# Performance work log

Hardware: AMD Instinct MI355X
Metric: run time of the kernel (lower is better)

Reference implementation:

```python
import jax, jax.numpy as jnp
import numpy as np

N_HEAD = 16
DIMS = 1024

def setup_inputs() -> dict:
    key = jax.random.key(0)
    ks = jax.random.split(key, 5)
    B, T, C = 4, 2048, DIMS
    std = 1.0 / np.sqrt(C)
    x = jax.random.normal(ks[0], (B, T, C), dtype=jnp.float32)
    W_attn = jax.random.normal(ks[1], (C, 3 * C), dtype=jnp.float32) * std
    b_attn = jnp.zeros((3 * C,), dtype=jnp.float32)
    W_proj = jax.random.normal(ks[2], (C, C), dtype=jnp.float32) * std
    b_proj = jnp.zeros((C,), dtype=jnp.float32)
    return {"x": x, "W_attn": W_attn, "b_attn": b_attn, "W_proj": W_proj, "b_proj": b_proj}

def reference(x, W_attn, b_attn, W_proj, b_proj):
    B, T, C = x.shape
    H = N_HEAD
    D = C // H
    qkv = x @ W_attn + b_attn  # [B,T,3C]
    q, k, v = jnp.split(qkv, 3, axis=-1)
    # [B,T,C] -> [B,H,T,D]
    q = q.reshape(B, T, H, D).transpose(0, 2, 1, 3)
    k = k.reshape(B, T, H, D).transpose(0, 2, 1, 3)
    v = v.reshape(B, T, H, D).transpose(0, 2, 1, 3)
    att = jnp.einsum('bhqd,bhkd->bhqk', q, k) * (1.0 / np.sqrt(D))
    causal = jnp.tril(jnp.ones((T, T), dtype=bool))  # [T,T]
    att = jnp.where(causal[None, None, :, :], att, -jnp.inf)
    att = jax.nn.softmax(att, axis=-1)
    # dropout p=0.0 -> identity in eval/zero-prob mode
    y = jnp.einsum('bhqk,bhkd->bhqd', att, v)  # [B,H,T,D]
    y = y.transpose(0, 2, 1, 3).reshape(B, T, C)
    y = y @ W_proj + b_proj
    return y
```

## Files before the change

kernel.cpp:

```cpp
#include <hip/hip_runtime.h>
#include <hip/hip_bf16.h>
#include <stdint.h>

typedef unsigned short u16;
typedef unsigned int   u32;

using short8 = __attribute__((ext_vector_type(8))) short;
using f32x4  = __attribute__((ext_vector_type(4))) float;

__device__ __forceinline__ float b2f(u32 u) {
    union { u32 i; float f; } v;
    v.i = u << 16;
    return v.f;
}
__device__ __forceinline__ u16 f2b(float f) {
    union { float f; u32 i; } v; v.f = f;
    u32 x = v.i;
    x += 0x7fffu + ((x >> 16) & 1u);
    return (u16)(x >> 16);
}
__device__ __forceinline__ u32 pkbf16(float lo, float hi) {
    __hip_bfloat162 h = __float22bfloat162_rn(float2{lo, hi});
    return *reinterpret_cast<u32*>(&h);
}
__device__ __forceinline__ float fexp2(float x) {
#if __has_builtin(__builtin_amdgcn_exp2f)
    return __builtin_amdgcn_exp2f(x);
#else
    return exp2f(x);
#endif
}
__device__ __forceinline__ u32 perm_lo(u32 a, u32 b) {
#if __has_builtin(__builtin_amdgcn_perm)
    return __builtin_amdgcn_perm(b, a, 0x05040100u);
#else
    return (a & 0xffffu) | (b << 16);
#endif
}
__device__ __forceinline__ u32 perm_hi(u32 a, u32 b) {
#if __has_builtin(__builtin_amdgcn_perm)
    return __builtin_amdgcn_perm(b, a, 0x07060302u);
#else
    return (a >> 16) | (b & 0xffff0000u);
#endif
}

__device__ __forceinline__ void gll16(const u16* g, u16* l) {
    __builtin_amdgcn_global_load_lds(
        (const __attribute__((address_space(1))) void*)g,
        (__attribute__((address_space(3))) void*)l, 16, 0, 0);
}

__global__ __launch_bounds__(256)
void cast_bf16(const float* __restrict__ in, u16* __restrict__ out, int n)
{
    const int i = (blockIdx.x * 256 + threadIdx.x) * 8;
    if (i >= n) return;
    const float4 a = *reinterpret_cast<const float4*>(in + i);
    const float4 b = *reinterpret_cast<const float4*>(in + i + 4);
    *reinterpret_cast<uint4*>(out + i) = make_uint4(
        pkbf16(a.x, a.y), pkbf16(a.z, a.w), pkbf16(b.x, b.y), pkbf16(b.z, b.w));
}

__global__ __launch_bounds__(256)
void transpose_cast(const float* __restrict__ W, u16* __restrict__ Wt, int R, int Ncols)
{
    __shared__ float t[32][33];
    const int c0 = blockIdx.x * 32, r0 = blockIdx.y * 32;
    const int lx = threadIdx.x & 31, ly = threadIdx.x >> 5;
#pragma unroll
    for (int i = 0; i < 4; i++) {
        const int r = ly + i * 8;
        t[r][lx] = W[(size_t)(r0 + r) * Ncols + c0 + lx];
    }
    __syncthreads();
#pragma unroll
    for (int i = 0; i < 4; i++) {
        const int c = ly + i * 8;
        Wt[(size_t)(c0 + c) * R + r0 + lx] = f2b(t[lx][c]);
    }
}

template<typename OT>
__global__ __launch_bounds__(256)
void gemm_mfma(const u16* __restrict__ A, const u16* __restrict__ Bt,
               const float* __restrict__ bias, OT* __restrict__ C,
               int M, int N, int K)
{
    __shared__ u16 As[128 * 32];
    __shared__ u16 Bs[128 * 32];

    const int tid  = threadIdx.x;
    const int w    = tid >> 6;
    const int lane = tid & 63;
    const int quad = lane >> 4;
    const int c16  = lane & 15;
    const int wr   = w >> 1, wc = w & 1;

    const int m0 = blockIdx.y * 128;
    const int n0 = blockIdx.x * 128;

    const int srow = w * 32 + (lane >> 2);
    const int skc  = (lane & 3) * 8;
    const u16* gA = A  + (size_t)(m0 + srow) * K + skc;
    const u16* gB = Bt + (size_t)(n0 + srow) * K + skc;
    u16* lA = As + w * 32 * 32 + lane * 8;
    u16* lB = Bs + w * 32 * 32 + lane * 8;

    f32x4 acc[4][4];
#pragma unroll
    for (int i = 0; i < 4; i++)
#pragma unroll
        for (int j = 0; j < 4; j++) acc[i][j] = (f32x4){0.f, 0.f, 0.f, 0.f};

    for (int k0 = 0; k0 < K; k0 += 32) {
        __syncthreads();
        gll16(gA + k0,                  lA);
        gll16(gA + k0 + 16 * (size_t)K, lA + 16 * 32);
        gll16(gB + k0,                  lB);
        gll16(gB + k0 + 16 * (size_t)K, lB + 16 * 32);
        __syncthreads();

        short8 af[4], bf[4];
#pragma unroll
        for (int i = 0; i < 4; i++)
            af[i] = *reinterpret_cast<const short8*>(&As[(wr * 64 + i * 16 + c16) * 32 + quad * 8]);
#pragma unroll
        for (int j = 0; j < 4; j++)
            bf[j] = *reinterpret_cast<const short8*>(&Bs[(wc * 64 + j * 16 + c16) * 32 + quad * 8]);
#pragma unroll
        for (int i = 0; i < 4; i++)
#pragma unroll
            for (int j = 0; j < 4; j++)
                acc[i][j] = __builtin_amdgcn_mfma_f32_16x16x32_bf16(af[i], bf[j], acc[i][j], 0, 0, 0);
    }

#pragma unroll
    for (int i = 0; i < 4; i++)
#pragma unroll
        for (int j = 0; j < 4; j++) {
            const int colg = n0 + wc * 64 + j * 16 + c16;
            const float bv = bias[colg];
#pragma unroll
            for (int r = 0; r < 4; r++) {
                const int rowg = m0 + wr * 64 + i * 16 + quad * 4 + r;
                const float v = acc[i][j][r] + bv;
                if constexpr (sizeof(OT) == 2)
                    ((u16*)C)[(size_t)rowg * N + colg] = f2b(v);
                else
                    ((float*)C)[(size_t)rowg * N + colg] = v;
            }
        }
}

__global__ __launch_bounds__(512, 2)
void gemm_mfma_256(const u16* __restrict__ A, const u16* __restrict__ Bt,
                   const float* __restrict__ bias, u16* __restrict__ C,
                   int M, int N, int K)
{
    __shared__ u16 ring[4 * 16384];

    const int tid  = threadIdx.x;
    const int w    = tid >> 6;
    const int lane = tid & 63;
    const int quad = lane >> 4;
    const int c16  = lane & 15;
    const int wr   = w >> 2;
    const int wc   = w & 3;

    const int nwg  = gridDim.x * gridDim.y;
    const int orig = blockIdx.y * gridDim.x + blockIdx.x;
    const int swz  = (orig & 7) * (nwg >> 3) + (orig >> 3);
    const int bx   = swz % gridDim.x;
    const int by   = swz / gridDim.x;
    const int m0   = by * 256, n0 = bx * 256;

    const int r0s = w * 16 + (lane >> 2);
    const int qs  = (lane & 3) ^ ((r0s >> 1) & 3);
    const u16* gA = A  + (size_t)(m0 + r0s) * K + qs * 8;
    const u16* gB = Bt + (size_t)(n0 + r0s) * K + qs * 8;
    const size_t hstep = (size_t)128 * K;
    u16* dstB = ring + w * 512 + lane * 8;

    const int slot = quad ^ ((c16 >> 1) & 3);
    const int aoff = (wr * 128 + c16) * 32 + slot * 8;
    const int boff = 8192 + (wc * 64 + c16) * 32 + slot * 8;

    f32x4 acc[8][4];
#pragma unroll
    for (int i = 0; i < 8; i++)
#pragma unroll
        for (int j = 0; j < 4; j++) acc[i][j] = (f32x4){0.f, 0.f, 0.f, 0.f};

    const int nt = K >> 5;

#pragma unroll
    for (int t = 0; t < 3; t++) {
        u16* db = dstB + t * 16384;
        const size_t ko = (size_t)t * 32;
        gll16(gA + ko,         db);
        gll16(gA + ko + hstep, db + 4096);
        gll16(gB + ko,         db + 8192);
        gll16(gB + ko + hstep, db + 12288);
    }

#pragma unroll 1
    for (int t = 0; t < nt; t++) {
        const int remain = nt - 1 - t;
        if (remain >= 2)      asm volatile("s_waitcnt vmcnt(8)" ::: "memory");
        else if (remain == 1) asm volatile("s_waitcnt vmcnt(4)" ::: "memory");
        else                  asm volatile("s_waitcnt vmcnt(0)" ::: "memory");
        asm volatile("s_barrier" ::: "memory");

        const u16* buf = ring + (t & 3) * 16384;
        const bool pf  = (t + 3) < nt;
        u16* db = dstB + ((t + 3) & 3) * 16384;
        const size_t ko = (size_t)(t + 3) * 32;

        short8 bfr[4], afr[4];

#pragma unroll
        for (int j = 0; j < 4; j++)
            bfr[j] = *reinterpret_cast<const short8*>(buf + boff + j * 512);
#pragma unroll
        for (int i = 0; i < 4; i++)
            afr[i] = *reinterpret_cast<const short8*>(buf + aoff + i * 512);
        if (pf) { gll16(gA + ko, db); gll16(gA + ko + hstep, db + 4096); }
        asm volatile("s_waitcnt lgkmcnt(0)" ::: "memory");
        __builtin_amdgcn_sched_barrier(0);
        __builtin_amdgcn_s_setprio(1);
#pragma unroll
        for (int i = 0; i < 4; i++)
#pragma unroll
            for (int j = 0; j < 4; j++)
                acc[i][j] = __builtin_amdgcn_mfma_f32_16x16x32_bf16(afr[i], bfr[j], acc[i][j], 0, 0, 0);
        __builtin_amdgcn_s_setprio(0);
        asm volatile("s_barrier" ::: "memory");

#pragma unroll
        for (int i = 0; i < 4; i++)
            afr[i] = *reinterpret_cast<const short8*>(buf + aoff + (i + 4) * 512);
        if (pf) { gll16(gB + ko, db + 8192); gll16(gB + ko + hstep, db + 12288); }
        asm volatile("s_waitcnt lgkmcnt(0)" ::: "memory");
        __builtin_amdgcn_sched_barrier(0);
        __builtin_amdgcn_s_setprio(1);
#pragma unroll
        for (int i = 0; i < 4; i++)
#pragma unroll
            for (int j = 0; j < 4; j++)
                acc[i + 4][j] = __builtin_amdgcn_mfma_f32_16x16x32_bf16(afr[i], bfr[j], acc[i + 4][j], 0, 0, 0);
        __builtin_amdgcn_s_setprio(0);
        asm volatile("s_barrier" ::: "memory");
    }

#pragma unroll
    for (int i = 0; i < 8; i++)
#pragma unroll
        for (int j = 0; j < 4; j++) {
            const int colg = n0 + wc * 64 + j * 16 + c16;
            const float bv = bias[colg];
#pragma unroll
            for (int r = 0; r < 4; r++) {
                const int rowg = m0 + wr * 128 + i * 16 + quad * 4 + r;
                C[(size_t)rowg * N + colg] = f2b(acc[i][j][r] + bv);
            }
        }
}

constexpr int ALDP = 72;

struct TileState {
    f32x4 O[4];
    float m, l;
    short8 qf[2];
    int qglob;
};

__device__ __forceinline__ void tile_pass(
    const u16 (*__restrict__ Ks)[ALDP], const u16 (*__restrict__ Vt)[ALDP],
    u16* __restrict__ plrow,
    TileState& ts, int kt0, bool diag, int quad, int c16)
{
    f32x4 s[4];
#pragma unroll
    for (int sub = 0; sub < 4; sub++) {
        short8 kf0 = *reinterpret_cast<const short8*>(&Ks[sub * 16 + c16][0 * 32 + quad * 8]);
        short8 kf1 = *reinterpret_cast<const short8*>(&Ks[sub * 16 + c16][1 * 32 + quad * 8]);
        f32x4 acc = (f32x4){0.f, 0.f, 0.f, 0.f};
        acc = __builtin_amdgcn_mfma_f32_16x16x32_bf16(kf0, ts.qf[0], acc, 0, 0, 0);
        acc = __builtin_amdgcn_mfma_f32_16x16x32_bf16(kf1, ts.qf[1], acc, 0, 0, 0);
        s[sub] = acc;
    }

    if (diag) {
#pragma unroll
        for (int sub = 0; sub < 4; sub++)
#pragma unroll
            for (int r = 0; r < 4; r++)
                if (kt0 + sub * 16 + quad * 4 + r > ts.qglob) s[sub][r] = -INFINITY;
    }

    float mloc = -INFINITY;
#pragma unroll
    for (int sub = 0; sub < 4; sub++)
#pragma unroll
        for (int r = 0; r < 4; r++) mloc = fmaxf(mloc, s[sub][r]);
    mloc = fmaxf(mloc, __shfl_xor(mloc, 16));
    mloc = fmaxf(mloc, __shfl_xor(mloc, 32));
    const float mnew = fmaxf(ts.m, mloc);
    const float al   = fexp2(ts.m - mnew);
    ts.m = mnew;

    float ls = 0.f;
#pragma unroll
    for (int sub = 0; sub < 4; sub++) {
#pragma unroll
        for (int r = 0; r < 4; r++) {
            s[sub][r] = fexp2(s[sub][r] - mnew);
            ls += s[sub][r];
        }
        *reinterpret_cast<uint2*>(plrow + c16 * ALDP + sub * 16 + quad * 4) =
            make_uint2(pkbf16(s[sub][0], s[sub][1]), pkbf16(s[sub][2], s[sub][3]));
    }
    ls += __shfl_xor(ls, 16);
    ls += __shfl_xor(ls, 32);
    ts.l = ts.l * al + ls;

#pragma unroll
    for (int r = 0; r < 4; r++) {
        const float alr = __shfl(al, quad * 4 + r);
#pragma unroll
        for (int d = 0; d < 4; d++) ts.O[d][r] *= alr;
    }

    short8 pf[2];
#pragma unroll
    for (int c = 0; c < 2; c++)
        pf[c] = *reinterpret_cast<const short8*>(plrow + c16 * ALDP + c * 32 + quad * 8);

#pragma unroll
    for (int dsub = 0; dsub < 4; dsub++) {
#pragma unroll
        for (int c = 0; c < 2; c++) {
            short8 vf = *reinterpret_cast<const short8*>(&Vt[dsub * 16 + c16][c * 32 + quad * 8]);
            ts.O[dsub] = __builtin_amdgcn_mfma_f32_16x16x32_bf16(pf[c], vf, ts.O[dsub], 0, 0, 0);
        }
    }
}

__global__ __launch_bounds__(256)
void attn_flash(const u16* __restrict__ qkv, u16* __restrict__ out)
{
    constexpr int T = 2048, C = 1024, C3 = 3072;

    __shared__ u16 Ks[64][ALDP];
    __shared__ u16 Vt[64][ALDP];
    __shared__ u16 Pl[4][16][ALDP];

    const int tid  = threadIdx.x;
    const int w    = tid >> 6;
    const int lane = tid & 63;
    const int quad = lane >> 4;
    const int c16  = lane & 15;

    const int qtA = blockIdx.x;
    const int qtB = 31 - qtA;
    const int bh  = blockIdx.y;
    const int h   = bh & 15;
    const int b   = bh >> 4;

    const int kr  = tid >> 2, kc = (tid & 3) * 16;
    const int vkp = tid & 31, vdg = (tid >> 5) * 8;
    const u16* baseK = qkv + (size_t)(b * T + kr) * C3 + C + h * 64 + kc;
    const u16* baseV = qkv + (size_t)(b * T + 2 * vkp) * C3 + 2 * C + h * 64 + vdg;

    u16* plrow = &Pl[w][0][0];

#pragma unroll 1
    for (int phase = 0; phase < 2; ++phase) {
        const int qt = phase ? qtA : qtB;

        TileState ts;
        ts.qglob = qt * 64 + w * 16 + c16;
        ts.m = -INFINITY;
        ts.l = 0.f;
#pragma unroll
        for (int d = 0; d < 4; d++) ts.O[d] = (f32x4){0.f, 0.f, 0.f, 0.f};
        constexpr float QSCALE = 0.125f * 1.44269504089f;
#pragma unroll
        for (int c = 0; c < 2; c++) {
            short8 rq = *reinterpret_cast<const short8*>(
                qkv + (size_t)(b * T + ts.qglob) * C3 + h * 64 + c * 32 + quad * 8);
#pragma unroll
            for (int j = 0; j < 8; j++)
                ts.qf[c][j] = (short)f2b(b2f((u16)rq[j]) * QSCALE);
        }

        for (int kt = 0; kt <= qt; kt++) {
            const int kt0 = kt * 64;
            __syncthreads();
            {
                const uint4* gp = reinterpret_cast<const uint4*>(baseK + (size_t)kt0 * C3);
                uint4 ka = gp[0], kb = gp[1];
                const u16* g0 = baseV + (size_t)kt0 * C3;
                uint4 va = *reinterpret_cast<const uint4*>(g0);
                uint4 vb = *reinterpret_cast<const uint4*>(g0 + C3);
                *reinterpret_cast<uint4*>(&Ks[kr][kc])     = ka;
                *reinterpret_cast<uint4*>(&Ks[kr][kc + 8]) = kb;
                const u32* aw = reinterpret_cast<const u32*>(&va);
                const u32* bw = reinterpret_cast<const u32*>(&vb);
#pragma unroll
                for (int i = 0; i < 4; i++) {
                    *reinterpret_cast<u32*>(&Vt[vdg + 2 * i][2 * vkp])     = perm_lo(aw[i], bw[i]);
                    *reinterpret_cast<u32*>(&Vt[vdg + 2 * i + 1][2 * vkp]) = perm_hi(aw[i], bw[i]);
                }
            }
            __syncthreads();

            tile_pass(Ks, Vt, plrow, ts, kt0, kt == qt, quad, c16);
        }

        const float inv = 1.0f / ts.l;
#pragma unroll
        for (int r = 0; r < 4; r++) {
            const float invr = __shfl(inv, quad * 4 + r);
            const int qrow = qt * 64 + w * 16 + quad * 4 + r;
#pragma unroll
            for (int dsub = 0; dsub < 4; dsub++)
                out[(size_t)(b * T + qrow) * C + h * 64 + dsub * 16 + c16] =
                    f2b(ts.O[dsub][r] * invr);
        }
    }
}

extern "C" void kernel_launch(void* const* d_in, const int* in_sizes, int n_in,
                              void* d_out, int out_size, void* d_ws, size_t ws_size,
                              hipStream_t stream)
{
    constexpr int B = 4, T = 2048, C = 1024;
    constexpr int M = B * T;
    const float* x      = (const float*)d_in[0];
    const float* W_attn = (const float*)d_in[1];
    const float* b_attn = (const float*)d_in[2];
    const float* W_proj = (const float*)d_in[3];
    const float* b_proj = (const float*)d_in[4];
    float* out = (float*)d_out;

    char* p = (char*)d_ws;
    u16* qkv     = (u16*)p;                 p += (size_t)M * 3 * C * sizeof(u16);
    u16* xb      = (u16*)p;
    u16* attn_o  = (u16*)p;                 p += (size_t)M * C * sizeof(u16);
    u16* Wt_attn = (u16*)p;                 p += (size_t)3 * C * C * sizeof(u16);
    u16* Wt_proj = (u16*)p;

    cast_bf16<<<dim3(M * C / (256 * 8)), 256, 0, stream>>>(x, xb, M * C);
    transpose_cast<<<dim3(3 * C / 32, C / 32), 256, 0, stream>>>(W_attn, Wt_attn, C, 3 * C);
    transpose_cast<<<dim3(C / 32, C / 32), 256, 0, stream>>>(W_proj, Wt_proj, C, C);

    gemm_mfma_256<<<dim3(3 * C / 256, M / 256), 512, 0, stream>>>(
        xb, Wt_attn, b_attn, qkv, M, 3 * C, C);

    attn_flash<<<dim3(16, B * 16), 256, 0, stream>>>(qkv, attn_o);

    gemm_mfma<float><<<dim3(C / 128, M / 128), 256, 0, stream>>>(
        attn_o, Wt_proj, b_proj, out, M, C, C);
}
```

Measured before the change: 290.3 us.

## Prefetch K/V tiles, add lazy softmax rescale, and stage GEMM epilogue via LDS

The attention loop now loads the next K/V tile from global memory into registers while the current tile is being computed, so load latency overlaps the MFMA work. The online softmax skips rescaling O and l unless the running max rises by more than 8 (in log2 units), which removes multiplies and shuffles on most tiles at a small cost in numeric headroom. MFMA sections get raised wave priority. The GEMM epilogue writes each output sub-tile into an LDS ring buffer and then stores coalesced 16-byte vectors, adding two barriers per row group.

```diff
diff --git a/kernel.cpp b/kernel.cpp
--- a/kernel.cpp
+++ b/kernel.cpp
@@ -253,18 +253,30 @@
         asm volatile("s_barrier" ::: "memory");
     }
 
-#pragma unroll
-    for (int i = 0; i < 8; i++)
-#pragma unroll
-        for (int j = 0; j < 4; j++) {
-            const int colg = n0 + wc * 64 + j * 16 + c16;
-            const float bv = bias[colg];
-#pragma unroll
-            for (int r = 0; r < 4; r++) {
-                const int rowg = m0 + wr * 128 + i * 16 + quad * 4 + r;
-                C[(size_t)rowg * N + colg] = f2b(acc[i][j][r] + bv);
-            }
-        }
+    float bv[4];
+#pragma unroll
+    for (int j = 0; j < 4; j++) bv[j] = bias[n0 + wc * 64 + j * 16 + c16];
+
+    const int erow = wr * 16 + quad * 4;
+    const int ecol = wc * 64 + c16;
+#pragma unroll
+    for (int i = 0; i < 8; i++) {
+#pragma unroll
+        for (int j = 0; j < 4; j++)
+#pragma unroll
+            for (int r = 0; r < 4; r++)
+                ring[(erow + r) * 264 + ecol + j * 16] = f2b(acc[i][j][r] + bv[j]);
+        __syncthreads();
+#pragma unroll
+        for (int rr = 0; rr < 2; rr++) {
+            const int lr = rr * 16 + (tid >> 5);
+            const int cc = (tid & 31) * 8;
+            const uint4 vvec = *reinterpret_cast<const uint4*>(&ring[lr * 264 + cc]);
+            const int gr = m0 + (lr >> 4) * 128 + i * 16 + (lr & 15);
+            *reinterpret_cast<uint4*>(&C[(size_t)gr * N + n0 + cc]) = vvec;
+        }
+        __syncthreads();
+    }
 }
 
 constexpr int ALDP = 72;
@@ -282,6 +294,7 @@
     TileState& ts, int kt0, bool diag, int quad, int c16)
 {
     f32x4 s[4];
+    __builtin_amdgcn_s_setprio(1);
 #pragma unroll
     for (int sub = 0; sub < 4; sub++) {
         short8 kf0 = *reinterpret_cast<const short8*>(&Ks[sub * 16 + c16][0 * 32 + quad * 8]);
@@ -291,6 +304,7 @@
         acc = __builtin_amdgcn_mfma_f32_16x16x32_bf16(kf1, ts.qf[1], acc, 0, 0, 0);
         s[sub] = acc;
     }
+    __builtin_amdgcn_s_setprio(0);
 
     if (diag) {
 #pragma unroll
@@ -300,44 +314,46 @@
                 if (kt0 + sub * 16 + quad * 4 + r > ts.qglob) s[sub][r] = -INFINITY;
     }
 
-    float mloc = -INFINITY;
-#pragma unroll
-    for (int sub = 0; sub < 4; sub++)
-#pragma unroll
-        for (int r = 0; r < 4; r++) mloc = fmaxf(mloc, s[sub][r]);
+    float m0a = fmaxf(fmaxf(s[0][0], s[0][1]), fmaxf(s[0][2], s[0][3]));
+    float m1a = fmaxf(fmaxf(s[1][0], s[1][1]), fmaxf(s[1][2], s[1][3]));
+    float m2a = fmaxf(fmaxf(s[2][0], s[2][1]), fmaxf(s[2][2], s[2][3]));
+    float m3a = fmaxf(fmaxf(s[3][0], s[3][1]), fmaxf(s[3][2], s[3][3]));
+    float mloc = fmaxf(fmaxf(m0a, m1a), fmaxf(m2a, m3a));
     mloc = fmaxf(mloc, __shfl_xor(mloc, 16));
     mloc = fmaxf(mloc, __shfl_xor(mloc, 32));
-    const float mnew = fmaxf(ts.m, mloc);
-    const float al   = fexp2(ts.m - mnew);
-    ts.m = mnew;
+
+    if (!__all(mloc <= ts.m + 8.f)) {
+        const float mnew = fmaxf(ts.m, mloc);
+        const float al   = fexp2(ts.m - mnew);
+        ts.m = mnew;
+        ts.l *= al;
+#pragma unroll
+        for (int r = 0; r < 4; r++) {
+            const float alr = __shfl(al, quad * 4 + r);
+#pragma unroll
+            for (int d = 0; d < 4; d++) ts.O[d][r] *= alr;
+        }
+    }
 
     float ls = 0.f;
 #pragma unroll
     for (int sub = 0; sub < 4; sub++) {
 #pragma unroll
-        for (int r = 0; r < 4; r++) {
-            s[sub][r] = fexp2(s[sub][r] - mnew);
-            ls += s[sub][r];
-        }
+        for (int r = 0; r < 4; r++) s[sub][r] = fexp2(s[sub][r] - ts.m);
+        ls += (s[sub][0] + s[sub][1]) + (s[sub][2] + s[sub][3]);
         *reinterpret_cast<uint2*>(plrow + c16 * ALDP + sub * 16 + quad * 4) =
             make_uint2(pkbf16(s[sub][0], s[sub][1]), pkbf16(s[sub][2], s[sub][3]));
     }
     ls += __shfl_xor(ls, 16);
     ls += __shfl_xor(ls, 32);
-    ts.l = ts.l * al + ls;
-
-#pragma unroll
-    for (int r = 0; r < 4; r++) {
-        const float alr = __shfl(al, quad * 4 + r);
-#pragma unroll
-        for (int d = 0; d < 4; d++) ts.O[d][r] *= alr;
-    }
+    ts.l += ls;
 
     short8 pf[2];
 #pragma unroll
     for (int c = 0; c < 2; c++)
         pf[c] = *reinterpret_cast<const short8*>(plrow + c16 * ALDP + c * 32 + quad * 8);
 
+    __builtin_amdgcn_s_setprio(1);
 #pragma unroll
     for (int dsub = 0; dsub < 4; dsub++) {
 #pragma unroll
@@ -346,6 +362,7 @@
             ts.O[dsub] = __builtin_amdgcn_mfma_f32_16x16x32_bf16(pf[c], vf, ts.O[dsub], 0, 0, 0);
         }
     }
+    __builtin_amdgcn_s_setprio(0);
 }
 
 __global__ __launch_bounds__(256)
@@ -376,6 +393,8 @@
 
     u16* plrow = &Pl[w][0][0];
 
+    uint4 ka, kb, va, vb;
+
 #pragma unroll 1
     for (int phase = 0; phase < 2; ++phase) {
         const int qt = phase ? qtA : qtB;
@@ -396,17 +415,19 @@
                 ts.qf[c][j] = (short)f2b(b2f((u16)rq[j]) * QSCALE);
         }
 
+        {
+            const uint4* gp = reinterpret_cast<const uint4*>(baseK);
+            ka = gp[0]; kb = gp[1];
+            va = *reinterpret_cast<const uint4*>(baseV);
+            vb = *reinterpret_cast<const uint4*>(baseV + C3);
+        }
+
         for (int kt = 0; kt <= qt; kt++) {
             const int kt0 = kt * 64;
             __syncthreads();
+            *reinterpret_cast<uint4*>(&Ks[kr][kc])     = ka;
+            *reinterpret_cast<uint4*>(&Ks[kr][kc + 8]) = kb;
             {
-                const uint4* gp = reinterpret_cast<const uint4*>(baseK + (size_t)kt0 * C3);
-                uint4 ka = gp[0], kb = gp[1];
-                const u16* g0 = baseV + (size_t)kt0 * C3;
-                uint4 va = *reinterpret_cast<const uint4*>(g0);
-                uint4 vb = *reinterpret_cast<const uint4*>(g0 + C3);
-                *reinterpret_cast<uint4*>(&Ks[kr][kc])     = ka;
-                *reinterpret_cast<uint4*>(&Ks[kr][kc + 8]) = kb;
                 const u32* aw = reinterpret_cast<const u32*>(&va);
                 const u32* bw = reinterpret_cast<const u32*>(&vb);
 #pragma unroll
@@ -416,6 +437,15 @@
                 }
             }
             __syncthreads();
+
+            if (kt < qt) {
+                const int nk0 = (kt + 1) * 64;
+                const uint4* gp = reinterpret_cast<const uint4*>(baseK + (size_t)nk0 * C3);
+                ka = gp[0]; kb = gp[1];
+                const u16* g0 = baseV + (size_t)nk0 * C3;
+                va = *reinterpret_cast<const uint4*>(g0);
+                vb = *reinterpret_cast<const uint4*>(g0 + C3);
+            }
 
             tile_pass(Ks, Vt, plrow, ts, kt0, kt == qt, quad, c16);
         }
```

After: 278.2 us. -4.1%, faster.
